# Optimization experiments

Measured on AMD Instinct MI355X. Metric: run time of the kernel, lower is better.

The kernel has to match this reference:

```python
import jax, jax.numpy as jnp
import numpy as np

N_USERS = 8000
N_ENTITIES = 32000
EMB = 64
N_HOPS = 2
N_GROUPS = 4
N_EDGES = 200000
TAU = 0.5


def _l2norm(x):
    # F.normalize(x, p=2, dim=1): x / max(||x||_2, eps)
    n = jnp.sqrt(jnp.sum(x * x, axis=1, keepdims=True))
    return x / jnp.maximum(n, 1e-12)


def setup_inputs() -> dict:
    key = jax.random.key(0)
    ks = jax.random.split(key, 8)
    return {
        "user_emb": jax.random.normal(ks[0], (N_USERS, EMB), jnp.float32),
        "user_ui_emb": jax.random.normal(ks[1], (N_USERS, EMB), jnp.float32),
        "entity_emb": jax.random.normal(ks[2], (N_ENTITIES, EMB), jnp.float32),
        "W1": jax.random.normal(ks[3], (EMB, EMB), jnp.float32) * 0.05,
        "b1": jnp.zeros((EMB,), jnp.float32),
        "W2": jax.random.normal(ks[4], (EMB, EMB), jnp.float32) * 0.05,
        "b2": jnp.zeros((EMB,), jnp.float32),
        "ui_index": jax.random.randint(ks[5], (N_GROUPS, N_EDGES), 0, N_USERS),
        "ei_index": jax.random.randint(ks[6], (N_GROUPS, N_EDGES), 0, N_ENTITIES),
        "mess_dropout": 0,  # eval mode: dropout disabled for deterministic reference
    }


def reference(user_emb, user_ui_emb, entity_emb, W1, b1, W2, b2,
              ui_index, ei_index, mess_dropout):
    accs = []    # per-group accumulated user embeddings
    scores = []  # per-group attention logits
    for g in range(N_GROUPS):
        ui = ui_index[g]  # [E] user index per edge
        ei = ei_index[g]  # [E] entity index per edge
        u_agg = user_emb
        e_int = entity_emb
        acc = jnp.zeros_like(user_emb)
        for _hop in range(N_HOPS):
            u_prev = u_agg
            u_msg = e_int[ei]   # gather entity->user messages per edge [E, D]
            e_msg = u_prev[ui]  # gather user->entity messages per edge [E, D]
            u_agg = jax.ops.segment_sum(u_msg, ui, num_segments=N_USERS)
            e_int = jax.ops.segment_sum(e_msg, ei, num_segments=N_ENTITIES)
            # mess_dropout == 0 in this reference (eval mode), so dropout is identity
            u_agg = _l2norm(u_agg)
            e_int = _l2norm(e_int)
            acc = acc + u_agg
        accs.append(acc)
        scores.append(jnp.sum(acc * user_ui_emb, axis=1))

    acc_stack = jnp.stack(accs, axis=1)                     # [U, G, D]
    att = jax.nn.softmax(jnp.stack(scores, axis=1), axis=1)  # [U, G]
    user_int_emb = jnp.sum(acc_stack * att[..., None], axis=1) + user_emb

    # Contrast_user: 2-layer ELU projection, cosine-sim InfoNCE at temperature tau
    def proj(z):
        return jax.nn.elu(z @ W1 + b1) @ W2 + b2

    p1 = _l2norm(proj(user_ui_emb))
    p2 = _l2norm(proj(user_int_emb))
    logits = (p1 @ p2.T) / TAU                              # [U, U]
    l12 = -jnp.diag(jax.nn.log_softmax(logits, axis=1))
    l21 = -jnp.diag(jax.nn.log_softmax(logits.T, axis=1))
    user_cl_loss = 0.5 * (jnp.mean(l12) + jnp.mean(l21))

    return (user_int_emb, user_cl_loss)
```

## Files before the change

### kernel.cpp

```cpp
#include <hip/hip_runtime.h>
#include <hip/hip_bf16.h>
#include <math.h>

#define N_USERS 8000
#define N_ENTITIES 32000
#define EMB 64
#define N_GROUPS 4
#define N_EDGES 200000

#define UBUCK 500
#define EBUCK 1000
#define UCAP 640
#define ECAP 384
#define BIN_CHUNK 2048

typedef __attribute__((ext_vector_type(8))) __bf16 bf16x8;
typedef __attribute__((ext_vector_type(16))) float f32x16;

static __device__ __forceinline__ unsigned short f2bf(float f) {
    union { float f; unsigned int i; } x; x.f = f;
    return (unsigned short)((x.i + 0x7FFF + ((x.i >> 16) & 1)) >> 16);
}
static __device__ __forceinline__ float u2f(unsigned int u) {
    union { unsigned int i; float f; } x; x.i = u; return x.f;
}

__global__ __launch_bounds__(256) void convert_tables(
    const float* __restrict__ ue, const float* __restrict__ ee,
    ushort* __restrict__ ueh, ushort* __restrict__ eeh)
{
    int i4 = blockIdx.x * 256 + threadIdx.x;
    if (i4 < 128000) {
        float4 v = ((const float4*)ue)[i4];
        ushort4 o; o.x = f2bf(v.x); o.y = f2bf(v.y); o.z = f2bf(v.z); o.w = f2bf(v.w);
        ((ushort4*)ueh)[i4] = o;
    } else if (i4 < 640000) {
        int j = i4 - 128000;
        float4 v = ((const float4*)ee)[j];
        ushort4 o; o.x = f2bf(v.x); o.y = f2bf(v.y); o.z = f2bf(v.z); o.w = f2bf(v.w);
        ((ushort4*)eeh)[j] = o;
    }
}

__global__ __launch_bounds__(256) void bin_edges(
    const int* __restrict__ ui_index, const int* __restrict__ ei_index,
    int* __restrict__ cnt_u, int* __restrict__ cnt_e,
    int* __restrict__ bin_u, int* __restrict__ bin_e)
{
    int g = blockIdx.y;
    const int* ui = ui_index + (size_t)g * N_EDGES;
    const int* ei = ei_index + (size_t)g * N_EDGES;
    __shared__ int hU[UBUCK], hE[EBUCK], bU[UBUCK], bE[EBUCK];
    int t = threadIdx.x;
    for (int i = t; i < UBUCK; i += 256) hU[i] = 0;
    for (int i = t; i < EBUCK; i += 256) hE[i] = 0;
    __syncthreads();
    int e0 = blockIdx.x * BIN_CHUNK;
    int us[8], vs[8];
    #pragma unroll
    for (int i = 0; i < 8; ++i) {
        int e = e0 + i * 256 + t;
        bool ok = e < N_EDGES;
        us[i] = ok ? ui[e] : -1;
        vs[i] = ok ? ei[e] : 0;
        if (ok) {
            atomicAdd(&hU[us[i] >> 4], 1);
            atomicAdd(&hE[vs[i] >> 5], 1);
        }
    }
    __syncthreads();
    for (int i = t; i < UBUCK; i += 256) {
        int c = hU[i];
        bU[i] = c ? atomicAdd(&cnt_u[g * UBUCK + i], c) : 0;
        hU[i] = 0;
    }
    for (int i = t; i < EBUCK; i += 256) {
        int c = hE[i];
        bE[i] = c ? atomicAdd(&cnt_e[g * EBUCK + i], c) : 0;
        hE[i] = 0;
    }
    __syncthreads();
    #pragma unroll
    for (int i = 0; i < 8; ++i) {
        if (us[i] >= 0) {
            int bu = us[i] >> 4;
            int s = atomicAdd(&hU[bu], 1) + bU[bu];
            if (s < UCAP)
                bin_u[((size_t)g * UBUCK + bu) * UCAP + s] = (us[i] & 15) | (vs[i] << 4);
            int be = vs[i] >> 5;
            int s2 = atomicAdd(&hE[be], 1) + bE[be];
            if (s2 < ECAP)
                bin_e[((size_t)g * EBUCK + be) * ECAP + s2] = (vs[i] & 31) | (us[i] << 5);
        }
    }
}

static __device__ __forceinline__ void map_gb(int gbase, int affin, int& g, int& b)
{
    if (affin) {
        int bid = blockIdx.x;
        int xcd = bid & 7;
        g = xcd >> 1;
        b = ((bid >> 3) << 1) | (xcd & 1);
    } else {
        g = gbase + blockIdx.y;
        b = blockIdx.x;
    }
}

__global__ __launch_bounds__(256) void agg_entity_b(
    const int* __restrict__ cnt_e, const int* __restrict__ bin_e,
    const ushort* __restrict__ ueh, ushort* __restrict__ ebufh,
    int gbase, int affin)
{
    int g, b;
    map_gb(gbase, affin, g, b);
    int gz = g - gbase;
    __shared__ int wds[ECAP];
    __shared__ int srt[ECAP];
    __shared__ int cnt[32];
    __shared__ int ptr[33];
    __shared__ int cur[32];
    int t = threadIdx.x;
    int count = min(cnt_e[g * EBUCK + b], ECAP);
    const int* bin = bin_e + ((size_t)g * EBUCK + b) * ECAP;
    if (t < 32) cnt[t] = 0;
    __syncthreads();
    for (int i = t; i < count; i += 256) {
        int w_ = bin[i];
        wds[i] = w_;
        atomicAdd(&cnt[w_ & 31], 1);
    }
    __syncthreads();
    if (t == 0) {
        int run = 0;
        for (int i = 0; i < 32; ++i) { ptr[i] = run; run += cnt[i]; }
        ptr[32] = run;
    }
    __syncthreads();
    if (t < 32) cur[t] = ptr[t];
    __syncthreads();
    for (int i = t; i < count; i += 256) {
        int w_ = wds[i];
        int pos = atomicAdd(&cur[w_ & 31], 1);
        srt[pos] = w_ >> 5;
    }
    __syncthreads();
    int wv = t >> 6, lane = t & 63, q = lane >> 4, d16 = lane & 15;
    for (int r = wv; r < 32; r += 4) {
        int start = ptr[r], end = ptr[r + 1];
        float a0 = 0.f, a1 = 0.f, a2 = 0.f, a3 = 0.f;
        for (int base = start; base < end; base += 4) {
            int idx = base + q;
            int src = idx < end ? srt[idx] : -1;
            unsigned sidx = src >= 0 ? (unsigned)src : 0u;
            uint2 r2 = *(const uint2*)(ueh + (sidx << 6) + (d16 << 2));
            if (src < 0) { r2.x = 0u; r2.y = 0u; }
            a0 += u2f(r2.x << 16);
            a1 += u2f(r2.x & 0xFFFF0000u);
            a2 += u2f(r2.y << 16);
            a3 += u2f(r2.y & 0xFFFF0000u);
        }
        a0 += __shfl_xor(a0, 16); a0 += __shfl_xor(a0, 32);
        a1 += __shfl_xor(a1, 16); a1 += __shfl_xor(a1, 32);
        a2 += __shfl_xor(a2, 16); a2 += __shfl_xor(a2, 32);
        a3 += __shfl_xor(a3, 16); a3 += __shfl_xor(a3, 32);
        float ss = a0 * a0 + a1 * a1 + a2 * a2 + a3 * a3;
        #pragma unroll
        for (int off = 1; off < 16; off <<= 1) ss += __shfl_xor(ss, off);
        float inv = 1.0f / fmaxf(sqrtf(ss), 1e-12f);
        if (lane < 16) {
            ushort4 o;
            o.x = f2bf(a0 * inv); o.y = f2bf(a1 * inv);
            o.z = f2bf(a2 * inv); o.w = f2bf(a3 * inv);
            *(ushort4*)(ebufh + (size_t)gz * N_ENTITIES * EMB
                        + (((size_t)b * 32 + r) << 6) + (d16 << 2)) = o;
        }
    }
}

__global__ __launch_bounds__(256) void agg_user_b(
    const int* __restrict__ cnt_u, const int* __restrict__ bin_u,
    const ushort* __restrict__ eeh, const ushort* __restrict__ ebufh,
    float* __restrict__ acc, int gbase, int affin)
{
    int g, b;
    map_gb(gbase, affin, g, b);
    int gz = g - gbase;
    __shared__ int wds[UCAP];
    __shared__ int srt[UCAP];
    __shared__ int cnt[16];
    __shared__ int ptr[17];
    __shared__ int cur[16];
    int t = threadIdx.x;
    int count = min(cnt_u[g * UBUCK + b], UCAP);
    const int* bin = bin_u + ((size_t)g * UBUCK + b) * UCAP;
    const ushort* tabB = ebufh + (size_t)gz * N_ENTITIES * EMB;
    if (t < 16) cnt[t] = 0;
    __syncthreads();
    for (int i = t; i < count; i += 256) {
        int w_ = bin[i];
        wds[i] = w_;
        atomicAdd(&cnt[w_ & 15], 1);
    }
    __syncthreads();
    if (t == 0) {
        int run = 0;
        for (int i = 0; i < 16; ++i) { ptr[i] = run; run += cnt[i]; }
        ptr[16] = run;
    }
    __syncthreads();
    if (t < 16) cur[t] = ptr[t];
    __syncthreads();
    for (int i = t; i < count; i += 256) {
        int w_ = wds[i];
        int pos = atomicAdd(&cur[w_ & 15], 1);
        srt[pos] = w_ >> 4;
    }
    __syncthreads();
    int wv = t >> 6, lane = t & 63, q = lane >> 4, d16 = lane & 15;
    for (int r = wv; r < 16; r += 4) {
        int start = ptr[r], end = ptr[r + 1];
        float a0 = 0.f, a1 = 0.f, a2 = 0.f, a3 = 0.f;
        float b0 = 0.f, b1_ = 0.f, b2_ = 0.f, b3 = 0.f;
        for (int base = start; base < end; base += 4) {
            int idx = base + q;
            int src = idx < end ? srt[idx] : -1;
            unsigned sidx = src >= 0 ? (unsigned)src : 0u;
            unsigned off = (sidx << 6) + (d16 << 2);
            uint2 ra = *(const uint2*)(eeh + off);
            uint2 rb = *(const uint2*)(tabB + off);
            if (src < 0) { ra.x = 0u; ra.y = 0u; rb.x = 0u; rb.y = 0u; }
            a0 += u2f(ra.x << 16);
            a1 += u2f(ra.x & 0xFFFF0000u);
            a2 += u2f(ra.y << 16);
            a3 += u2f(ra.y & 0xFFFF0000u);
            b0  += u2f(rb.x << 16);
            b1_ += u2f(rb.x & 0xFFFF0000u);
            b2_ += u2f(rb.y << 16);
            b3  += u2f(rb.y & 0xFFFF0000u);
        }
        a0 += __shfl_xor(a0, 16); a0 += __shfl_xor(a0, 32);
        a1 += __shfl_xor(a1, 16); a1 += __shfl_xor(a1, 32);
        a2 += __shfl_xor(a2, 16); a2 += __shfl_xor(a2, 32);
        a3 += __shfl_xor(a3, 16); a3 += __shfl_xor(a3, 32);
        b0  += __shfl_xor(b0, 16);  b0  += __shfl_xor(b0, 32);
        b1_ += __shfl_xor(b1_, 16); b1_ += __shfl_xor(b1_, 32);
        b2_ += __shfl_xor(b2_, 16); b2_ += __shfl_xor(b2_, 32);
        b3  += __shfl_xor(b3, 16);  b3  += __shfl_xor(b3, 32);
        float ssA = a0 * a0 + a1 * a1 + a2 * a2 + a3 * a3;
        float ssB = b0 * b0 + b1_ * b1_ + b2_ * b2_ + b3 * b3;
        #pragma unroll
        for (int off = 1; off < 16; off <<= 1) {
            ssA += __shfl_xor(ssA, off);
            ssB += __shfl_xor(ssB, off);
        }
        float invA = 1.0f / fmaxf(sqrtf(ssA), 1e-12f);
        float invB = 1.0f / fmaxf(sqrtf(ssB), 1e-12f);
        if (lane < 16) {
            float4 o;
            o.x = a0 * invA + b0 * invB;
            o.y = a1 * invA + b1_ * invB;
            o.z = a2 * invA + b2_ * invB;
            o.w = a3 * invA + b3 * invB;
            *(float4*)(acc + (size_t)g * N_USERS * EMB
                       + (((size_t)b * 16 + r) << 6) + (d16 << 2)) = o;
        }
    }
}

__global__ __launch_bounds__(256) void combine_proj(
    const float* __restrict__ acc, const float* __restrict__ uie,
    const float* __restrict__ uemb,
    const float* __restrict__ W1, const float* __restrict__ b1,
    const float* __restrict__ W2, const float* __restrict__ b2,
    float* __restrict__ out_user,
    ushort* __restrict__ p1h, ushort* __restrict__ p2h,
    float* __restrict__ diag)
{
    __shared__ float W1s[EMB * EMB];
    __shared__ float W2s[EMB * EMB];
    __shared__ float zs[4][2][EMB];
    __shared__ float hs[4][2][EMB];
    int t = threadIdx.x;
    for (int i = t; i < EMB * EMB; i += 256) { W1s[i] = W1[i]; W2s[i] = W2[i]; }
    int w = t >> 6, lane = t & 63;
    int u = blockIdx.x * 4 + w;

    float ue = uie[(u << 6) + lane];
    float av[N_GROUPS], s[N_GROUPS];
    #pragma unroll
    for (int g = 0; g < N_GROUPS; ++g) {
        av[g] = acc[(size_t)g * N_USERS * EMB + (u << 6) + lane];
        float p = av[g] * ue;
        #pragma unroll
        for (int off = 1; off < 64; off <<= 1) p += __shfl_xor(p, off);
        s[g] = p;
    }
    float m = fmaxf(fmaxf(s[0], s[1]), fmaxf(s[2], s[3]));
    float att[N_GROUPS], tot = 0.f;
    #pragma unroll
    for (int g = 0; g < N_GROUPS; ++g) { att[g] = __expf(s[g] - m); tot += att[g]; }
    float inv = 1.0f / tot;
    float o = uemb[(u << 6) + lane];
    #pragma unroll
    for (int g = 0; g < N_GROUPS; ++g) o += att[g] * inv * av[g];
    out_user[(u << 6) + lane] = o;

    zs[w][0][lane] = ue;
    zs[w][1][lane] = o;
    __syncthreads();
    float h0 = b1[lane], h1 = b1[lane];
    #pragma unroll
    for (int k = 0; k < EMB; ++k) {
        float w1 = W1s[k * EMB + lane];
        h0 = fmaf(zs[w][0][k], w1, h0);
        h1 = fmaf(zs[w][1][k], w1, h1);
    }
    h0 = h0 > 0.f ? h0 : expm1f(h0);
    h1 = h1 > 0.f ? h1 : expm1f(h1);
    hs[w][0][lane] = h0;
    hs[w][1][lane] = h1;
    __syncthreads();
    float y0 = b2[lane], y1 = b2[lane];
    #pragma unroll
    for (int k = 0; k < EMB; ++k) {
        float w2 = W2s[k * EMB + lane];
        y0 = fmaf(hs[w][0][k], w2, y0);
        y1 = fmaf(hs[w][1][k], w2, y1);
    }
    float ss0 = y0 * y0, ss1 = y1 * y1;
    #pragma unroll
    for (int off = 1; off < 64; off <<= 1) {
        ss0 += __shfl_xor(ss0, off);
        ss1 += __shfl_xor(ss1, off);
    }
    float n0 = y0 / fmaxf(sqrtf(ss0), 1e-12f);
    float n1 = y1 / fmaxf(sqrtf(ss1), 1e-12f);
    p1h[(u << 6) + lane] = f2bf(n0);
    p2h[(u << 6) + lane] = f2bf(n1);
    float d = n0 * n1;
    #pragma unroll
    for (int off = 1; off < 64; off <<= 1) d += __shfl_xor(d, off);
    if (lane == 0) diag[u] = d * 2.0f;
}

#define NCHUNK 50
__global__ __launch_bounds__(256) void lse_tile(
    const ushort* __restrict__ Ah, const ushort* __restrict__ Bh,
    float* __restrict__ rowp, float* __restrict__ colp)
{
    __shared__ ushort Bs[160 * 68];
    int t = threadIdx.x;
    int cb = blockIdx.x % 50;
    int rb = blockIdx.x / 50;
    int j0 = cb * 160;
    for (int slot = t; slot < 1280; slot += 256) {
        int row = slot >> 3;
        int o8 = (slot & 7) << 3;
        uint4 v = *(const uint4*)(Bh + (size_t)(j0 + row) * 64 + o8);
        ushort* dst = Bs + row * 68 + o8;
        *(uint2*)(dst + 0) = make_uint2(v.x, v.y);
        *(uint2*)(dst + 4) = make_uint2(v.z, v.w);
    }
    __syncthreads();
    int w = t >> 6, lane = t & 63;
    int strip = rb * 4 + w;
    if (strip >= 250) return;
    int i0 = strip * 32;
    int hl = lane >> 5, l31 = lane & 31;

    const bf16x8* A8 = (const bf16x8*)Ah;
    bf16x8 afrag[4];
    #pragma unroll
    for (int m = 0; m < 4; ++m)
        afrag[m] = A8[(i0 + l31) * 8 + m * 2 + hl];

    float rowacc[16];
    #pragma unroll
    for (int r = 0; r < 16; ++r) rowacc[r] = 0.f;

    #pragma unroll
    for (int cs = 0; cs < 5; ++cs) {
        bf16x8 bfrag[4];
        #pragma unroll
        for (int m = 0; m < 4; ++m) {
            const ushort* p = Bs + (cs * 32 + l31) * 68 + m * 16 + hl * 8;
            union { uint2 u[2]; bf16x8 f; } cv;
            cv.u[0] = *(const uint2*)p;
            cv.u[1] = *(const uint2*)(p + 4);
            bfrag[m] = cv.f;
        }
        f32x16 acc;
        #pragma unroll
        for (int r = 0; r < 16; ++r) acc[r] = 0.f;
        #pragma unroll
        for (int m = 0; m < 4; ++m)
            acc = __builtin_amdgcn_mfma_f32_32x32x16_bf16(afrag[m], bfrag[m], acc, 0, 0, 0);
        float e[16];
        #pragma unroll
        for (int r = 0; r < 16; ++r) {
            e[r] = __expf(acc[r] * 2.0f);
            rowacc[r] += e[r];
        }
        float c01 = (e[0] + e[1]) + (e[2] + e[3]);
        float c23 = (e[4] + e[5]) + (e[6] + e[7]);
        float c45 = (e[8] + e[9]) + (e[10] + e[11]);
        float c67 = (e[12] + e[13]) + (e[14] + e[15]);
        float csum = (c01 + c23) + (c45 + c67);
        csum += __shfl_xor(csum, 32);
        if (lane < 32) colp[strip * 8000 + j0 + cs * 32 + lane] = csum;
    }
    #pragma unroll
    for (int r = 0; r < 16; ++r) {
        float v = rowacc[r];
        #pragma unroll
        for (int off = 1; off < 32; off <<= 1) v += __shfl_xor(v, off);
        if (l31 == 0)
            rowp[cb * 8000 + i0 + (r & 3) + 8 * (r >> 2) + 4 * hl] = v;
    }
}

__global__ __launch_bounds__(256) void reduce_partials(
    const float* __restrict__ rowp, const float* __restrict__ colp,
    float* __restrict__ se_row, float* __restrict__ se_col)
{
    int id = blockIdx.x * 256 + threadIdx.x;
    if (id < N_USERS) {
        float s = 0.f;
        for (int c = 0; c < NCHUNK; ++c) s += rowp[c * 8000 + id];
        se_row[id] = s;
    } else if (id < 2 * N_USERS) {
        int j = id - N_USERS;
        float s = 0.f;
        for (int st = 0; st < 250; ++st) s += colp[st * 8000 + j];
        se_col[j] = s;
    }
}

__global__ __launch_bounds__(256) void loss_kernel(
    const float* __restrict__ se_row, const float* __restrict__ se_col,
    const float* __restrict__ diag, float* __restrict__ out)
{
    __shared__ float red[256];
    int t = threadIdx.x;
    float s = 0.f;
    for (int i = t; i < N_USERS; i += 256)
        s += 0.5f * (logf(se_row[i]) + logf(se_col[i])) - diag[i];
    red[t] = s;
    __syncthreads();
    for (int w = 128; w > 0; w >>= 1) {
        if (t < w) red[t] += red[t + w];
        __syncthreads();
    }
    if (t == 0) out[0] = red[0] / (float)N_USERS;
}

extern "C" void kernel_launch(void* const* d_in, const int* in_sizes, int n_in,
                              void* d_out, int out_size, void* d_ws, size_t ws_size,
                              hipStream_t stream)
{
    const float* user_emb   = (const float*)d_in[0];
    const float* user_ui    = (const float*)d_in[1];
    const float* entity_emb = (const float*)d_in[2];
    const float* W1 = (const float*)d_in[3];
    const float* b1 = (const float*)d_in[4];
    const float* W2 = (const float*)d_in[5];
    const float* b2 = (const float*)d_in[6];
    const int* ui_index = (const int*)d_in[7];
    const int* ei_index = (const int*)d_in[8];

    float* ws = (float*)d_ws;
    float* acc    = ws;
    float* colp   = acc;
    float* se_row = ws + 2048000;
    float* se_col = se_row + 8000;
    float* diag   = se_col + 8000;
    ushort* p1h = (ushort*)(ws + 2072000);
    ushort* p2h = (ushort*)(ws + 2328000);
    float* rowp = ws + 2584000;
    int* cnt_u = (int*)(ws + 2984000);
    int* cnt_e = cnt_u + N_GROUPS * UBUCK;
    int* bin_u = cnt_e + N_GROUPS * EBUCK;
    int* bin_e = bin_u + N_GROUPS * UBUCK * UCAP;
    ushort* ueh = (ushort*)(ws + 5806000);
    ushort* eeh = (ushort*)(ws + 6062000);
    ushort* ebufh = (ushort*)(ws + 7086000);

    const size_t BASE_F = 7086000;
    int nG = 1;
    if (ws_size >= (BASE_F + 4 * 1024000) * 4) nG = 4;
    else if (ws_size >= (BASE_F + 2 * 1024000) * 4) nG = 2;

    float* out_user = (float*)d_out;
    float* out_loss = out_user + 512000;

    dim3 b256(256);

    hipMemsetAsync(cnt_u, 0, (size_t)N_GROUPS * (UBUCK + EBUCK) * 4, stream);
    convert_tables<<<2500, b256, 0, stream>>>(user_emb, entity_emb, ueh, eeh);
    bin_edges<<<dim3((N_EDGES + BIN_CHUNK - 1) / BIN_CHUNK, N_GROUPS), b256, 0, stream>>>(
        ui_index, ei_index, cnt_u, cnt_e, bin_u, bin_e);

    if (nG == 4) {
        agg_entity_b<<<EBUCK * 4, b256, 0, stream>>>(
            cnt_e, bin_e, ueh, ebufh, 0, 1);
        agg_user_b<<<UBUCK * 4, b256, 0, stream>>>(
            cnt_u, bin_u, eeh, ebufh, acc, 0, 1);
    } else {
        for (int gbase = 0; gbase < N_GROUPS; gbase += nG) {
            agg_entity_b<<<dim3(EBUCK, nG), b256, 0, stream>>>(
                cnt_e, bin_e, ueh, ebufh, gbase, 0);
            agg_user_b<<<dim3(UBUCK, nG), b256, 0, stream>>>(
                cnt_u, bin_u, eeh, ebufh, acc, gbase, 0);
        }
    }

    combine_proj<<<N_USERS / 4, b256, 0, stream>>>(
        acc, user_ui, user_emb, W1, b1, W2, b2,
        out_user, p1h, p2h, diag);

    lse_tile<<<63 * 50, b256, 0, stream>>>(p1h, p2h, rowp, colp);
    reduce_partials<<<(2 * N_USERS + 255) / 256, b256, 0, stream>>>(
        rowp, colp, se_row, se_col);
    loss_kernel<<<1, b256, 0, stream>>>(se_row, se_col, diag, out_loss);
}
```

Baseline: 172.6 us.

## Parallel-scan bucket offsets, unroll gather loops, reduce column partials in-block

Swaps the serial single-thread prefix sum in both aggregation kernels for a wavefront shuffle scan. It also unrolls the edge-gather loops to issue two row loads per iteration, giving more memory-level parallelism. In the LSE tile kernel, the four waves' column partial sums are combined through shared memory before writing, so colp holds 63 row-blocks instead of 250 strips. That shrinks the column reduction in reduce_partials, at the cost of an extra block barrier and keeping dead waves alive until it.

```diff
diff --git a/kernel.cpp b/kernel.cpp
--- a/kernel.cpp
+++ b/kernel.cpp
@@ -13,6 +13,7 @@
 #define UCAP 640
 #define ECAP 384
 #define BIN_CHUNK 2048
+#define NRB 63
 
 typedef __attribute__((ext_vector_type(8))) __bf16 bf16x8;
 typedef __attribute__((ext_vector_type(16))) float f32x16;
@@ -132,13 +133,21 @@
         atomicAdd(&cnt[w_ & 31], 1);
     }
     __syncthreads();
-    if (t == 0) {
-        int run = 0;
-        for (int i = 0; i < 32; ++i) { ptr[i] = run; run += cnt[i]; }
-        ptr[32] = run;
-    }
-    __syncthreads();
-    if (t < 32) cur[t] = ptr[t];
+    if (t < 64) {
+        int lane = t;
+        int c = (lane < 32) ? cnt[lane] : 0;
+        int val = c;
+        #pragma unroll
+        for (int off = 1; off < 32; off <<= 1) {
+            int y = __shfl_up(val, off, 64);
+            if (lane >= off) val += y;
+        }
+        if (lane < 32) {
+            ptr[lane + 1] = val;
+            cur[lane] = val - c;
+            if (lane == 0) ptr[0] = 0;
+        }
+    }
     __syncthreads();
     for (int i = t; i < count; i += 256) {
         int w_ = wds[i];
@@ -150,12 +159,20 @@
     for (int r = wv; r < 32; r += 4) {
         int start = ptr[r], end = ptr[r + 1];
         float a0 = 0.f, a1 = 0.f, a2 = 0.f, a3 = 0.f;
-        for (int base = start; base < end; base += 4) {
-            int idx = base + q;
-            int src = idx < end ? srt[idx] : -1;
-            unsigned sidx = src >= 0 ? (unsigned)src : 0u;
-            uint2 r2 = *(const uint2*)(ueh + (sidx << 6) + (d16 << 2));
-            if (src < 0) { r2.x = 0u; r2.y = 0u; }
+        for (int base = start; base < end; base += 8) {
+            int i1 = base + q, i2 = base + 4 + q;
+            int s1 = i1 < end ? srt[i1] : -1;
+            int s2 = i2 < end ? srt[i2] : -1;
+            unsigned x1 = s1 >= 0 ? (unsigned)s1 : 0u;
+            unsigned x2 = s2 >= 0 ? (unsigned)s2 : 0u;
+            uint2 r1 = *(const uint2*)(ueh + (x1 << 6) + (d16 << 2));
+            uint2 r2 = *(const uint2*)(ueh + (x2 << 6) + (d16 << 2));
+            if (s1 < 0) { r1.x = 0u; r1.y = 0u; }
+            if (s2 < 0) { r2.x = 0u; r2.y = 0u; }
+            a0 += u2f(r1.x << 16);
+            a1 += u2f(r1.x & 0xFFFF0000u);
+            a2 += u2f(r1.y << 16);
+            a3 += u2f(r1.y & 0xFFFF0000u);
             a0 += u2f(r2.x << 16);
             a1 += u2f(r2.x & 0xFFFF0000u);
             a2 += u2f(r2.y << 16);
@@ -204,13 +221,21 @@
         atomicAdd(&cnt[w_ & 15], 1);
     }
     __syncthreads();
-    if (t == 0) {
-        int run = 0;
-        for (int i = 0; i < 16; ++i) { ptr[i] = run; run += cnt[i]; }
-        ptr[16] = run;
-    }
-    __syncthreads();
-    if (t < 16) cur[t] = ptr[t];
+    if (t < 64) {
+        int lane = t;
+        int c = (lane < 16) ? cnt[lane] : 0;
+        int val = c;
+        #pragma unroll
+        for (int off = 1; off < 16; off <<= 1) {
+            int y = __shfl_up(val, off, 64);
+            if (lane >= off) val += y;
+        }
+        if (lane < 16) {
+            ptr[lane + 1] = val;
+            cur[lane] = val - c;
+            if (lane == 0) ptr[0] = 0;
+        }
+    }
     __syncthreads();
     for (int i = t; i < count; i += 256) {
         int w_ = wds[i];
@@ -223,22 +248,26 @@
         int start = ptr[r], end = ptr[r + 1];
         float a0 = 0.f, a1 = 0.f, a2 = 0.f, a3 = 0.f;
         float b0 = 0.f, b1_ = 0.f, b2_ = 0.f, b3 = 0.f;
-        for (int base = start; base < end; base += 4) {
-            int idx = base + q;
-            int src = idx < end ? srt[idx] : -1;
-            unsigned sidx = src >= 0 ? (unsigned)src : 0u;
-            unsigned off = (sidx << 6) + (d16 << 2);
-            uint2 ra = *(const uint2*)(eeh + off);
-            uint2 rb = *(const uint2*)(tabB + off);
-            if (src < 0) { ra.x = 0u; ra.y = 0u; rb.x = 0u; rb.y = 0u; }
-            a0 += u2f(ra.x << 16);
-            a1 += u2f(ra.x & 0xFFFF0000u);
-            a2 += u2f(ra.y << 16);
-            a3 += u2f(ra.y & 0xFFFF0000u);
-            b0  += u2f(rb.x << 16);
-            b1_ += u2f(rb.x & 0xFFFF0000u);
-            b2_ += u2f(rb.y << 16);
-            b3  += u2f(rb.y & 0xFFFF0000u);
+        for (int base = start; base < end; base += 8) {
+            int i1 = base + q, i2 = base + 4 + q;
+            int s1 = i1 < end ? srt[i1] : -1;
+            int s2 = i2 < end ? srt[i2] : -1;
+            unsigned o1 = ((s1 >= 0 ? (unsigned)s1 : 0u) << 6) + (d16 << 2);
+            unsigned o2 = ((s2 >= 0 ? (unsigned)s2 : 0u) << 6) + (d16 << 2);
+            uint2 ra1 = *(const uint2*)(eeh + o1);
+            uint2 rb1 = *(const uint2*)(tabB + o1);
+            uint2 ra2 = *(const uint2*)(eeh + o2);
+            uint2 rb2 = *(const uint2*)(tabB + o2);
+            if (s1 < 0) { ra1.x = 0u; ra1.y = 0u; rb1.x = 0u; rb1.y = 0u; }
+            if (s2 < 0) { ra2.x = 0u; ra2.y = 0u; rb2.x = 0u; rb2.y = 0u; }
+            a0 += u2f(ra1.x << 16) + u2f(ra2.x << 16);
+            a1 += u2f(ra1.x & 0xFFFF0000u) + u2f(ra2.x & 0xFFFF0000u);
+            a2 += u2f(ra1.y << 16) + u2f(ra2.y << 16);
+            a3 += u2f(ra1.y & 0xFFFF0000u) + u2f(ra2.y & 0xFFFF0000u);
+            b0  += u2f(rb1.x << 16) + u2f(rb2.x << 16);
+            b1_ += u2f(rb1.x & 0xFFFF0000u) + u2f(rb2.x & 0xFFFF0000u);
+            b2_ += u2f(rb1.y << 16) + u2f(rb2.y << 16);
+            b3  += u2f(rb1.y & 0xFFFF0000u) + u2f(rb2.y & 0xFFFF0000u);
         }
         a0 += __shfl_xor(a0, 16); a0 += __shfl_xor(a0, 32);
         a1 += __shfl_xor(a1, 16); a1 += __shfl_xor(a1, 32);
@@ -351,6 +380,7 @@
     float* __restrict__ rowp, float* __restrict__ colp)
 {
     __shared__ ushort Bs[160 * 68];
+    __shared__ float cw[4][160];
     int t = threadIdx.x;
     int cb = blockIdx.x % 50;
     int rb = blockIdx.x / 50;
@@ -366,8 +396,8 @@
     __syncthreads();
     int w = t >> 6, lane = t & 63;
     int strip = rb * 4 + w;
-    if (strip >= 250) return;
-    int i0 = strip * 32;
+    bool alive = strip < 250;
+    int i0 = alive ? strip * 32 : 0;
     int hl = lane >> 5, l31 = lane & 31;
 
     const bf16x8* A8 = (const bf16x8*)Ah;
@@ -409,15 +439,21 @@
         float c67 = (e[12] + e[13]) + (e[14] + e[15]);
         float csum = (c01 + c23) + (c45 + c67);
         csum += __shfl_xor(csum, 32);
-        if (lane < 32) colp[strip * 8000 + j0 + cs * 32 + lane] = csum;
-    }
-    #pragma unroll
-    for (int r = 0; r < 16; ++r) {
-        float v = rowacc[r];
-        #pragma unroll
-        for (int off = 1; off < 32; off <<= 1) v += __shfl_xor(v, off);
-        if (l31 == 0)
-            rowp[cb * 8000 + i0 + (r & 3) + 8 * (r >> 2) + 4 * hl] = v;
+        if (!alive) csum = 0.f;
+        if (lane < 32) cw[w][cs * 32 + lane] = csum;
+    }
+    __syncthreads();
+    if (t < 160)
+        colp[rb * 8000 + j0 + t] = (cw[0][t] + cw[1][t]) + (cw[2][t] + cw[3][t]);
+    if (alive) {
+        #pragma unroll
+        for (int r = 0; r < 16; ++r) {
+            float v = rowacc[r];
+            #pragma unroll
+            for (int off = 1; off < 32; off <<= 1) v += __shfl_xor(v, off);
+            if (l31 == 0)
+                rowp[cb * 8000 + i0 + (r & 3) + 8 * (r >> 2) + 4 * hl] = v;
+        }
     }
 }
 
@@ -433,7 +469,7 @@
     } else if (id < 2 * N_USERS) {
         int j = id - N_USERS;
         float s = 0.f;
-        for (int st = 0; st < 250; ++st) s += colp[st * 8000 + j];
+        for (int rb = 0; rb < NRB; ++rb) s += colp[rb * 8000 + j];
         se_col[j] = s;
     }
 }
@@ -520,7 +556,7 @@
         acc, user_ui, user_emb, W1, b1, W2, b2,
         out_user, p1h, p2h, diag);
 
-    lse_tile<<<63 * 50, b256, 0, stream>>>(p1h, p2h, rowp, colp);
+    lse_tile<<<NRB * 50, b256, 0, stream>>>(p1h, p2h, rowp, colp);
     reduce_partials<<<(2 * N_USERS + 255) / 256, b256, 0, stream>>>(
         rowp, colp, se_row, se_col);
     loss_kernel<<<1, b256, 0, stream>>>(se_row, se_col, diag, out_loss);
```

Measured after the change: 163.4 us. 5.3% less time.
